# Performance work log

Hardware: AMD Instinct MI355X
Metric: run time of the kernel (lower is better)

Reference implementation:

```python
import jax, jax.numpy as jnp
import numpy as np

H, W = 96, 96
THRESHOLD = 0.9
C = 256

def setup_inputs() -> dict:
    key = jax.random.key(0)
    k1, k2 = jax.random.split(key)
    return {
        "feature_query": jax.random.normal(k1, (C, H, W), jnp.float32),
        "feature_projection": jax.random.normal(k2, (C, H, W), jnp.float32),
    }

def reference(feature_query, feature_projection):
    c = feature_query.shape[0]
    # flatten spatial dims -> [C, N]; L2-normalize each pixel's descriptor over channels
    q = feature_query.reshape(c, -1)
    p = feature_projection.reshape(c, -1)
    q = q / jnp.linalg.norm(q, axis=0, keepdims=True)
    p = p / jnp.linalg.norm(p, axis=0, keepdims=True)
    # cosine similarity matrix [N, M] (GEMM)
    sim = jnp.einsum('cn,cm->nm', q, p)
    col_max = jnp.argmax(sim, axis=0)   # [M] best query row per projection column
    row_max = jnp.argmax(sim, axis=1)   # [N] best projection column per query row
    j = jnp.arange(sim.shape[1])
    q_idx = col_max                      # candidate query index for each column j
    sim_vals = sim[q_idx, j]
    # mutual nearest-neighbor + threshold (fixed-shape boolean mask instead of
    # a data-dependent python list, for jit compatibility)
    mutual = (row_max[q_idx] == j) & (sim_vals > THRESHOLD)
    # oneDim2TwoDim: (idx // W, idx % W), valid only if div+1 < H
    q_div, q_mod = q_idx // W, q_idx % W
    p_div, p_mod = j // W, j % W
    valid = mutual & (q_div + 1 < H) & (p_div + 1 < H)
    return sim, valid, q_idx, q_div, q_mod, p_div, p_mod
```

## Files before the change

### kernel.cpp

```cpp
#include <hip/hip_runtime.h>
#include <hip/hip_fp16.h>

#define N_PIX 9216
#define CCH 256
#define W_ 96
#define H_ 96
#define BM 128
#define BN 128
#define BK 16
#define TM 8
#define TN 8

typedef _Float16 half8_t __attribute__((ext_vector_type(8)));
typedef float f32x4_t __attribute__((ext_vector_type(4)));

__device__ __forceinline__ unsigned int mono_enc(float f) {
    unsigned int u = __float_as_uint(f);
    return (u & 0x80000000u) ? ~u : (u | 0x80000000u);
}
__device__ __forceinline__ float mono_dec(unsigned int e) {
    return __uint_as_float((e & 0x80000000u) ? (e ^ 0x80000000u) : ~e);
}

__device__ __forceinline__ void gload_lds16(const uint4* g, uint4* lds) {
    __builtin_amdgcn_global_load_lds(
        (const __attribute__((address_space(1))) unsigned int*)g,
        (__attribute__((address_space(3))) unsigned int*)lds, 16, 0, 0);
}


__global__ __launch_bounds__(256) void norms_kernel(const float* __restrict__ Q,
                                                    const float* __restrict__ P,
                                                    float* __restrict__ invq,
                                                    float* __restrict__ invp) {
    int n = blockIdx.x * blockDim.x + threadIdx.x;
    if (n >= N_PIX) return;
    float sq = 0.f, sp = 0.f;
    for (int c = 0; c < CCH; ++c) {
        float a = Q[(size_t)c * N_PIX + n];
        float b = P[(size_t)c * N_PIX + n];
        sq = fmaf(a, a, sq);
        sp = fmaf(b, b, sp);
    }
    invq[n] = 1.0f / sqrtf(sq);
    invp[n] = 1.0f / sqrtf(sp);
}

__device__ __forceinline__ int local_row(int ty, int i) {
    return (i < 4) ? (ty * 4 + i) : (64 + ty * 4 + (i - 4));
}
__device__ __forceinline__ int local_col(int tx, int j) {
    return (j < 4) ? (tx * 4 + j) : (64 + tx * 4 + (j - 4));
}

__global__ __launch_bounds__(256) void gemm_kernel(const float* __restrict__ Q,
                                                   const float* __restrict__ P,
                                                   const float* __restrict__ invq,
                                                   const float* __restrict__ invp,
                                                   float* __restrict__ sim,
                                                   unsigned long long* __restrict__ row_best,
                                                   unsigned long long* __restrict__ col_best) {
    __shared__ union SH {
        struct { float A[BK][BM]; float B[BK][BN]; } t;
        unsigned long long red[16][128];
    } sh;

    const int tid = threadIdx.x;
    const int tx = tid & 15;
    const int ty = tid >> 4;
    const int n0 = blockIdx.y * BM;
    const int m0 = blockIdx.x * BN;

    float acc[TM][TN];
#pragma unroll
    for (int i = 0; i < TM; ++i)
#pragma unroll
        for (int j = 0; j < TN; ++j) acc[i][j] = 0.f;

    for (int kk = 0; kk < CCH; kk += BK) {
#pragma unroll
        for (int rep = 0; rep < 2; ++rep) {
            int idx = tid + rep * 256;
            int row = idx >> 5;
            int c4  = idx & 31;
            float4 av = *(const float4*)&Q[(size_t)(kk + row) * N_PIX + n0 + c4 * 4];
            float4 bv = *(const float4*)&P[(size_t)(kk + row) * N_PIX + m0 + c4 * 4];
            *(float4*)&sh.t.A[row][c4 * 4] = av;
            *(float4*)&sh.t.B[row][c4 * 4] = bv;
        }
        __syncthreads();
#pragma unroll
        for (int k = 0; k < BK; ++k) {
            float a[TM], b[TN];
            *(float4*)&a[0] = *(const float4*)&sh.t.A[k][ty * 4];
            *(float4*)&a[4] = *(const float4*)&sh.t.A[k][ty * 4 + 64];
            *(float4*)&b[0] = *(const float4*)&sh.t.B[k][tx * 4];
            *(float4*)&b[4] = *(const float4*)&sh.t.B[k][tx * 4 + 64];
#pragma unroll
            for (int i = 0; i < TM; ++i)
#pragma unroll
                for (int j = 0; j < TN; ++j)
                    acc[i][j] = fmaf(a[i], b[j], acc[i][j]);
        }
        __syncthreads();
    }

    float iq[TM], ip[TN];
#pragma unroll
    for (int i = 0; i < TM; ++i) iq[i] = invq[n0 + local_row(ty, i)];
#pragma unroll
    for (int j = 0; j < TN; ++j) ip[j] = invp[m0 + local_col(tx, j)];
#pragma unroll
    for (int i = 0; i < TM; ++i)
#pragma unroll
        for (int j = 0; j < TN; ++j) acc[i][j] *= iq[i] * ip[j];

#pragma unroll
    for (int i = 0; i < TM; ++i) {
        int n = n0 + local_row(ty, i);
        float4 v0 = make_float4(acc[i][0], acc[i][1], acc[i][2], acc[i][3]);
        float4 v1 = make_float4(acc[i][4], acc[i][5], acc[i][6], acc[i][7]);
        float* dst = &sim[(size_t)n * N_PIX + m0];
        *(float4*)(dst + tx * 4) = v0;
        *(float4*)(dst + 64 + tx * 4) = v1;
    }

#pragma unroll
    for (int i = 0; i < TM; ++i) {
        float best = acc[i][0]; int bj = 0;
#pragma unroll
        for (int j = 1; j < TN; ++j)
            if (acc[i][j] > best) { best = acc[i][j]; bj = j; }
        unsigned int gcol = (unsigned int)(m0 + local_col(tx, bj));
        sh.red[tx][local_row(ty, i)] =
            ((unsigned long long)mono_enc(best) << 32) | (unsigned long long)(0xFFFFFFFFu - gcol);
    }
    __syncthreads();
    if (tid < 128) {
        unsigned long long best = sh.red[0][tid];
#pragma unroll
        for (int x = 1; x < 16; ++x) {
            unsigned long long v = sh.red[x][tid];
            if (v > best) best = v;
        }
        atomicMax(&row_best[n0 + tid], best);
    }
    __syncthreads();

#pragma unroll
    for (int j = 0; j < TN; ++j) {
        float best = acc[0][j]; int bi = 0;
#pragma unroll
        for (int i = 1; i < TM; ++i)
            if (acc[i][j] > best) { best = acc[i][j]; bi = i; }
        unsigned int grow = (unsigned int)(n0 + local_row(ty, bi));
        sh.red[ty][local_col(tx, j)] =
            ((unsigned long long)mono_enc(best) << 32) | (unsigned long long)(0xFFFFFFFFu - grow);
    }
    __syncthreads();
    if (tid < 128) {
        unsigned long long best = sh.red[0][tid];
#pragma unroll
        for (int x = 1; x < 16; ++x) {
            unsigned long long v = sh.red[x][tid];
            if (v > best) best = v;
        }
        atomicMax(&col_best[m0 + tid], best);
    }
}


__device__ __forceinline__ unsigned int pack_pair(float x, float y, float& rx, float& ry) {
    __half hx = __float2half(x), hy = __float2half(y);
    rx = x - __half2float(hx);
    ry = y - __half2float(hy);
    return (unsigned int)__half_as_ushort(hx) | ((unsigned int)__half_as_ushort(hy) << 16);
}

__global__ __launch_bounds__(256) void prep_kernel(const float* __restrict__ Q,
                                                   const float* __restrict__ P,
                                                   uint4* __restrict__ qh,
                                                   uint4* __restrict__ ql,
                                                   uint4* __restrict__ ph,
                                                   uint4* __restrict__ pl,
                                                   float* __restrict__ invq,
                                                   float* __restrict__ invp) {
    __shared__ float rq[4][64];
    __shared__ float rp[4][64];
    const int lane = threadIdx.x & 63;
    const int band = threadIdx.x >> 6;
    const int n = blockIdx.x * 64 + lane;
    float sq = 0.f, sp = 0.f;
    for (int kb = band * 8; kb < band * 8 + 8; ++kb) {
        float a[8], b[8];
#pragma unroll
        for (int t = 0; t < 8; ++t) {
            a[t] = Q[(size_t)(kb * 8 + t) * N_PIX + n];
            b[t] = P[(size_t)(kb * 8 + t) * N_PIX + n];
        }
#pragma unroll
        for (int t = 0; t < 8; ++t) {
            sq = fmaf(a[t], a[t], sq);
            sp = fmaf(b[t], b[t], sp);
        }
        uint4 vqh, vql, vph, vpl;
        unsigned int* uqh = (unsigned int*)&vqh;
        unsigned int* uql = (unsigned int*)&vql;
        unsigned int* uph = (unsigned int*)&vph;
        unsigned int* upl = (unsigned int*)&vpl;
#pragma unroll
        for (int j = 0; j < 4; ++j) {
            float r0, r1;
            uqh[j] = pack_pair(a[2 * j], a[2 * j + 1], r0, r1);
            uql[j] = (unsigned int)__half_as_ushort(__float2half(r0))
                   | ((unsigned int)__half_as_ushort(__float2half(r1)) << 16);
            uph[j] = pack_pair(b[2 * j], b[2 * j + 1], r0, r1);
            upl[j] = (unsigned int)__half_as_ushort(__float2half(r0))
                   | ((unsigned int)__half_as_ushort(__float2half(r1)) << 16);
        }
        size_t o = (size_t)kb * N_PIX + n;
        qh[o] = vqh; ql[o] = vql; ph[o] = vph; pl[o] = vpl;
    }
    rq[band][lane] = sq;
    rp[band][lane] = sp;
    __syncthreads();
    if (threadIdx.x < 64) {
        float tq = rq[0][lane] + rq[1][lane] + rq[2][lane] + rq[3][lane];
        float tp = rp[0][lane] + rp[1][lane] + rp[2][lane] + rp[3][lane];
        invq[n] = 1.0f / sqrtf(tq);
        invp[n] = 1.0f / sqrtf(tp);
    }
}

__global__ __launch_bounds__(256, 2) void mfma_gemm_kernel(
        const uint4* __restrict__ QH, const uint4* __restrict__ QL,
        const uint4* __restrict__ PH, const uint4* __restrict__ PL,
        const float* __restrict__ invq, const float* __restrict__ invp,
        float* __restrict__ sim,
        unsigned long long* __restrict__ row_best,
        unsigned long long* __restrict__ col_best) {
    const unsigned int bid = blockIdx.x;
    const unsigned int xcd = bid & 7u;
    const unsigned int nbl = bid >> 3;
    const unsigned int gg  = nbl / 72u;
    const unsigned int rr  = nbl % 72u;
    const unsigned int by  = xcd * 9u + (rr >> 3);
    const unsigned int bx  = gg * 8u + (rr & 7u);

    const int tid = threadIdx.x;
    const int l  = tid & 63;
    const int w  = tid >> 6;
    const int rl = l & 15;
    const int kg = l >> 4;
    const int n0 = (int)by * 128;
    const int m0 = (int)bx * 128;
    const int r0 = n0 + (w >> 1) * 64;
    const int c0 = m0 + (w & 1) * 64;

    __shared__ union SH2 {
        uint4 stage[2][4][4][128];
        float st[4][16][68];
    } sh;

    const f32x4_t zero4 = {0.f, 0.f, 0.f, 0.f};
    f32x4_t acc[4][4];
#pragma unroll
    for (int i = 0; i < 4; ++i)
#pragma unroll
        for (int j = 0; j < 4; ++j) acc[i][j] = zero4;

    const uint4* gsrc = (w == 0) ? (QH + n0) : (w == 1) ? (QL + n0)
                      : (w == 2) ? (PH + m0) : (PL + m0);

#pragma unroll
    for (int kb = 0; kb < 4; ++kb)
#pragma unroll
        for (int h = 0; h < 2; ++h)
            gload_lds16(gsrc + (size_t)kb * N_PIX + h * 64 + l,
                        &sh.stage[0][w][kb][h * 64]);
    asm volatile("s_waitcnt vmcnt(0)" ::: "memory");
    __syncthreads();

    const int ar = (w >> 1) * 64 + rl;
    const int br = (w & 1) * 64 + rl;

    for (int s = 0; s < 8; ++s) {
        const int cur = s & 1;
        if (s < 7) {
            const uint4* gs = gsrc + (size_t)((s + 1) * 4) * N_PIX;
#pragma unroll
            for (int kb = 0; kb < 4; ++kb)
#pragma unroll
                for (int h = 0; h < 2; ++h)
                    gload_lds16(gs + (size_t)kb * N_PIX + h * 64 + l,
                                &sh.stage[cur ^ 1][w][kb][h * 64]);
        }
        half8_t ah[4], al4[4], bh4[4], bl4[4];
#pragma unroll
        for (int f = 0; f < 4; ++f) {
            ah[f]  = *(const half8_t*)&sh.stage[cur][0][kg][ar + f * 16];
            al4[f] = *(const half8_t*)&sh.stage[cur][1][kg][ar + f * 16];
            bh4[f] = *(const half8_t*)&sh.stage[cur][2][kg][br + f * 16];
            bl4[f] = *(const half8_t*)&sh.stage[cur][3][kg][br + f * 16];
        }
#pragma unroll
        for (int fr = 0; fr < 4; ++fr)
#pragma unroll
            for (int fc = 0; fc < 4; ++fc) {
                acc[fr][fc] = __builtin_amdgcn_mfma_f32_16x16x32_f16(ah[fr],  bh4[fc], acc[fr][fc], 0, 0, 0);
                acc[fr][fc] = __builtin_amdgcn_mfma_f32_16x16x32_f16(ah[fr],  bl4[fc], acc[fr][fc], 0, 0, 0);
                acc[fr][fc] = __builtin_amdgcn_mfma_f32_16x16x32_f16(al4[fr], bh4[fc], acc[fr][fc], 0, 0, 0);
            }
        asm volatile("s_waitcnt vmcnt(0)" ::: "memory");
        __syncthreads();
    }

    float iq[4][4];
#pragma unroll
    for (int fr = 0; fr < 4; ++fr) {
        const float4 v = *(const float4*)&invq[r0 + fr * 16 + kg * 4];
        iq[fr][0] = v.x; iq[fr][1] = v.y; iq[fr][2] = v.z; iq[fr][3] = v.w;
    }
    float ip[4];
#pragma unroll
    for (int fc = 0; fc < 4; ++fc) ip[fc] = invp[c0 + fc * 16 + rl];

#pragma unroll
    for (int fr = 0; fr < 4; ++fr)
#pragma unroll
        for (int fc = 0; fc < 4; ++fc)
#pragma unroll
            for (int j = 0; j < 4; ++j)
                acc[fr][fc][j] *= iq[fr][j] * ip[fc];

#pragma unroll
    for (int fr = 0; fr < 4; ++fr)
#pragma unroll
        for (int j = 0; j < 4; ++j) {
            float best = acc[fr][0][j];
            int bf = 0;
#pragma unroll
            for (int fc = 1; fc < 4; ++fc)
                if (acc[fr][fc][j] > best) { best = acc[fr][fc][j]; bf = fc; }
            const unsigned int gcol = (unsigned int)(c0 + bf * 16 + rl);
            unsigned long long key = ((unsigned long long)mono_enc(best) << 32)
                                   | (unsigned long long)(0xFFFFFFFFu - gcol);
#pragma unroll
            for (int m = 1; m < 16; m <<= 1) {
                unsigned long long o = __shfl_xor(key, m, 64);
                if (o > key) key = o;
            }
            if (rl == 0)
                atomicMax(&row_best[r0 + fr * 16 + kg * 4 + j], key);
        }

#pragma unroll
    for (int fc = 0; fc < 4; ++fc) {
        float best = acc[0][fc][0];
        unsigned int brow = (unsigned int)(r0 + kg * 4);
#pragma unroll
        for (int fr = 0; fr < 4; ++fr)
#pragma unroll
            for (int j = 0; j < 4; ++j) {
                float v = acc[fr][fc][j];
                unsigned int rr2 = (unsigned int)(r0 + fr * 16 + kg * 4 + j);
                if (v > best) { best = v; brow = rr2; }
            }
        unsigned long long key = ((unsigned long long)mono_enc(best) << 32)
                               | (unsigned long long)(0xFFFFFFFFu - brow);
#pragma unroll
        for (int m = 16; m < 64; m <<= 1) {
            unsigned long long o = __shfl_xor(key, m, 64);
            if (o > key) key = o;
        }
        if (kg == 0)
            atomicMax(&col_best[c0 + fc * 16 + rl], key);
    }

#pragma unroll
    for (int fr = 0; fr < 4; ++fr) {
        asm volatile("s_waitcnt lgkmcnt(0)" ::: "memory");
#pragma unroll
        for (int fc = 0; fc < 4; ++fc)
#pragma unroll
            for (int j = 0; j < 4; ++j)
                sh.st[w][kg * 4 + j][fc * 16 + rl] = acc[fr][fc][j];
        asm volatile("s_waitcnt lgkmcnt(0)" ::: "memory");
#pragma unroll
        for (int pass = 0; pass < 4; ++pass) {
            const int rowL = pass * 4 + kg;
            const f32x4_t v = *(const f32x4_t*)&sh.st[w][rowL][rl * 4];
            const int gr = r0 + fr * 16 + rowL;
            __builtin_nontemporal_store(v, (f32x4_t*)(sim + (size_t)gr * N_PIX + c0 + rl * 4));
        }
    }
}


__global__ __launch_bounds__(256) void epilogue_kernel(const unsigned long long* __restrict__ row_best,
                                                       const unsigned long long* __restrict__ col_best,
                                                       float* __restrict__ out) {
    int j = blockIdx.x * blockDim.x + threadIdx.x;
    if (j >= N_PIX) return;
    unsigned long long cb = col_best[j];
    unsigned int q_idx = 0xFFFFFFFFu - (unsigned int)(cb & 0xFFFFFFFFull);
    float simval = mono_dec((unsigned int)(cb >> 32));
    unsigned long long rb = row_best[q_idx];
    unsigned int rm = 0xFFFFFFFFu - (unsigned int)(rb & 0xFFFFFFFFull);
    bool mutual = (rm == (unsigned int)j) && (simval > 0.9f);
    int qd = (int)(q_idx / W_), qm = (int)(q_idx % W_);
    int pd = j / W_, pm = j % W_;
    bool valid = mutual && (qd + 1 < H_) && (pd + 1 < H_);
    size_t base = (size_t)N_PIX * N_PIX;
    out[base + 0 * (size_t)N_PIX + j] = valid ? 1.0f : 0.0f;
    out[base + 1 * (size_t)N_PIX + j] = (float)q_idx;
    out[base + 2 * (size_t)N_PIX + j] = (float)qd;
    out[base + 3 * (size_t)N_PIX + j] = (float)qm;
    out[base + 4 * (size_t)N_PIX + j] = (float)pd;
    out[base + 5 * (size_t)N_PIX + j] = (float)pm;
}

extern "C" void kernel_launch(void* const* d_in, const int* in_sizes, int n_in,
                              void* d_out, int out_size, void* d_ws, size_t ws_size,
                              hipStream_t stream) {
    const float* Q = (const float*)d_in[0];
    const float* P = (const float*)d_in[1];
    float* out = (float*)d_out;

    unsigned long long* row_best = (unsigned long long*)d_ws;
    unsigned long long* col_best = row_best + N_PIX;
    float* invq = (float*)(col_best + N_PIX);
    float* invp = invq + N_PIX;

    hipMemsetAsync(d_ws, 0, 2 * N_PIX * sizeof(unsigned long long), stream);

    const size_t base_bytes = 2 * N_PIX * sizeof(unsigned long long) + 2 * N_PIX * sizeof(float);
    const size_t arr_u4 = (size_t)(CCH / 8) * N_PIX;
    const size_t need = base_bytes + 4 * arr_u4 * sizeof(uint4);

    if (ws_size >= need) {
        uint4* qh = (uint4*)((char*)d_ws + base_bytes);
        uint4* ql = qh + arr_u4;
        uint4* ph = ql + arr_u4;
        uint4* pl = ph + arr_u4;

        prep_kernel<<<N_PIX / 64, 256, 0, stream>>>(Q, P, qh, ql, ph, pl, invq, invp);
        mfma_gemm_kernel<<<5184, 256, 0, stream>>>(qh, ql, ph, pl, invq, invp,
                                                   out, row_best, col_best);
    } else {
        norms_kernel<<<N_PIX / 256, 256, 0, stream>>>(Q, P, invq, invp);
        dim3 grid(N_PIX / BN, N_PIX / BM);
        gemm_kernel<<<grid, 256, 0, stream>>>(Q, P, invq, invp, out, row_best, col_best);
    }

    epilogue_kernel<<<N_PIX / 256, 256, 0, stream>>>(row_best, col_best, out);
}
```

Baseline: 467.9 us.

## Enlarge GEMM tiles to 192x192 with 8 waves and triple-buffered LDS staging

Grows the block tile from 128x128 to 192x192 and the block from 256 to 512 threads, with each wave computing a 48x96 sub-tile (3x6 MFMA fragments). Staging becomes a three-deep LDS ring with partial vmcnt waits, so two K-steps of global loads are in flight while computing. The block-to-XCD mapping and the grid size change to match. The aim is more data reuse per load and better overlap of loads with MFMA work, at the cost of more LDS, more registers per thread and a grid of 2304 blocks that may fill the CUs less evenly.

```diff
diff --git a/kernel.cpp b/kernel.cpp
--- a/kernel.cpp
+++ b/kernel.cpp
@@ -232,7 +232,7 @@
     }
 }
 
-__global__ __launch_bounds__(256, 2) void mfma_gemm_kernel(
+__global__ __launch_bounds__(512, 2) void mfma_gemm_kernel(
         const uint4* __restrict__ QH, const uint4* __restrict__ QL,
         const uint4* __restrict__ PH, const uint4* __restrict__ PL,
         const float* __restrict__ invq, const float* __restrict__ invp,
@@ -242,105 +242,119 @@
     const unsigned int bid = blockIdx.x;
     const unsigned int xcd = bid & 7u;
     const unsigned int nbl = bid >> 3;
-    const unsigned int gg  = nbl / 72u;
-    const unsigned int rr  = nbl % 72u;
-    const unsigned int by  = xcd * 9u + (rr >> 3);
-    const unsigned int bx  = gg * 8u + (rr & 7u);
+    const unsigned int g   = nbl >> 3;
+    const unsigned int ii  = nbl & 7u;
+    const unsigned int by  = xcd * 6u + g % 6u;
+    const unsigned int bx  = (g / 6u) * 8u + ii;
 
     const int tid = threadIdx.x;
     const int l  = tid & 63;
     const int w  = tid >> 6;
     const int rl = l & 15;
     const int kg = l >> 4;
-    const int n0 = (int)by * 128;
-    const int m0 = (int)bx * 128;
-    const int r0 = n0 + (w >> 1) * 64;
-    const int c0 = m0 + (w & 1) * 64;
+    const int wr = w >> 1;
+    const int wc = w & 1;
+    const int n0 = (int)by * 192;
+    const int m0 = (int)bx * 192;
+    const int r0 = n0 + wr * 48;
+    const int c0 = m0 + wc * 96;
 
     __shared__ union SH2 {
-        uint4 stage[2][4][4][128];
-        float st[4][16][68];
+        uint4 stage[3][4][4][192];
+        float st[8][16][108];
     } sh;
 
     const f32x4_t zero4 = {0.f, 0.f, 0.f, 0.f};
-    f32x4_t acc[4][4];
-#pragma unroll
-    for (int i = 0; i < 4; ++i)
-#pragma unroll
-        for (int j = 0; j < 4; ++j) acc[i][j] = zero4;
-
-    const uint4* gsrc = (w == 0) ? (QH + n0) : (w == 1) ? (QL + n0)
-                      : (w == 2) ? (PH + m0) : (PL + m0);
-
-#pragma unroll
-    for (int kb = 0; kb < 4; ++kb)
-#pragma unroll
-        for (int h = 0; h < 2; ++h)
-            gload_lds16(gsrc + (size_t)kb * N_PIX + h * 64 + l,
-                        &sh.stage[0][w][kb][h * 64]);
-    asm volatile("s_waitcnt vmcnt(0)" ::: "memory");
-    __syncthreads();
-
-    const int ar = (w >> 1) * 64 + rl;
-    const int br = (w & 1) * 64 + rl;
-
+    f32x4_t acc[3][6];
+#pragma unroll
+    for (int i = 0; i < 3; ++i)
+#pragma unroll
+        for (int j = 0; j < 6; ++j) acc[i][j] = zero4;
+
+    const int h3  = w >> 2;
+    const int arr = w & 3;
+    const uint4* gsrc = (arr == 0) ? (QH + n0) : (arr == 1) ? (QL + n0)
+                      : (arr == 2) ? (PH + m0) : (PL + m0);
+
+#define STAGE(step, buf)                                                        \
+    {                                                                           \
+        _Pragma("unroll")                                                       \
+        for (int i = 0; i < 6; ++i) {                                           \
+            const int rest = 2 * i + h3;                                        \
+            const int kb = rest & 3;                                            \
+            const int px0 = (rest >> 2) * 64;                                   \
+            gload_lds16(gsrc + (size_t)((step) * 4 + kb) * N_PIX + px0 + l,     \
+                        &sh.stage[buf][arr][kb][px0]);                          \
+        }                                                                       \
+    }
+
+    STAGE(0, 0)
+    STAGE(1, 1)
+    asm volatile("s_waitcnt vmcnt(6)" ::: "memory");
+    __builtin_amdgcn_s_barrier();
+    __builtin_amdgcn_sched_barrier(0);
+
+#pragma unroll
     for (int s = 0; s < 8; ++s) {
-        const int cur = s & 1;
-        if (s < 7) {
-            const uint4* gs = gsrc + (size_t)((s + 1) * 4) * N_PIX;
-#pragma unroll
-            for (int kb = 0; kb < 4; ++kb)
-#pragma unroll
-                for (int h = 0; h < 2; ++h)
-                    gload_lds16(gs + (size_t)kb * N_PIX + h * 64 + l,
-                                &sh.stage[cur ^ 1][w][kb][h * 64]);
-        }
-        half8_t ah[4], al4[4], bh4[4], bl4[4];
-#pragma unroll
-        for (int f = 0; f < 4; ++f) {
-            ah[f]  = *(const half8_t*)&sh.stage[cur][0][kg][ar + f * 16];
-            al4[f] = *(const half8_t*)&sh.stage[cur][1][kg][ar + f * 16];
-            bh4[f] = *(const half8_t*)&sh.stage[cur][2][kg][br + f * 16];
-            bl4[f] = *(const half8_t*)&sh.stage[cur][3][kg][br + f * 16];
-        }
-#pragma unroll
-        for (int fr = 0; fr < 4; ++fr)
-#pragma unroll
-            for (int fc = 0; fc < 4; ++fc) {
-                acc[fr][fc] = __builtin_amdgcn_mfma_f32_16x16x32_f16(ah[fr],  bh4[fc], acc[fr][fc], 0, 0, 0);
-                acc[fr][fc] = __builtin_amdgcn_mfma_f32_16x16x32_f16(ah[fr],  bl4[fc], acc[fr][fc], 0, 0, 0);
-                acc[fr][fc] = __builtin_amdgcn_mfma_f32_16x16x32_f16(al4[fr], bh4[fc], acc[fr][fc], 0, 0, 0);
+        const int cur = s % 3;
+        if (s < 6) STAGE(s + 2, (s + 2) % 3)
+
+        half8_t ah[3], al_[3], bh_[6], bl_[6];
+#pragma unroll
+        for (int f = 0; f < 3; ++f) {
+            ah[f]  = *(const half8_t*)&sh.stage[cur][0][kg][wr * 48 + f * 16 + rl];
+            al_[f] = *(const half8_t*)&sh.stage[cur][1][kg][wr * 48 + f * 16 + rl];
+        }
+#pragma unroll
+        for (int f = 0; f < 6; ++f) {
+            bh_[f] = *(const half8_t*)&sh.stage[cur][2][kg][wc * 96 + f * 16 + rl];
+            bl_[f] = *(const half8_t*)&sh.stage[cur][3][kg][wc * 96 + f * 16 + rl];
+        }
+#pragma unroll
+        for (int fr = 0; fr < 3; ++fr)
+#pragma unroll
+            for (int fc = 0; fc < 6; ++fc) {
+                acc[fr][fc] = __builtin_amdgcn_mfma_f32_16x16x32_f16(ah[fr],  bh_[fc], acc[fr][fc], 0, 0, 0);
+                acc[fr][fc] = __builtin_amdgcn_mfma_f32_16x16x32_f16(ah[fr],  bl_[fc], acc[fr][fc], 0, 0, 0);
+                acc[fr][fc] = __builtin_amdgcn_mfma_f32_16x16x32_f16(al_[fr], bh_[fc], acc[fr][fc], 0, 0, 0);
             }
-        asm volatile("s_waitcnt vmcnt(0)" ::: "memory");
-        __syncthreads();
-    }
-
-    float iq[4][4];
-#pragma unroll
-    for (int fr = 0; fr < 4; ++fr) {
+
+        if (s < 6) {
+            asm volatile("s_waitcnt vmcnt(6)" ::: "memory");
+        } else if (s == 6) {
+            asm volatile("s_waitcnt vmcnt(0)" ::: "memory");
+        }
+        __builtin_amdgcn_s_barrier();
+        __builtin_amdgcn_sched_barrier(0);
+    }
+#undef STAGE
+
+    float iq[3][4];
+#pragma unroll
+    for (int fr = 0; fr < 3; ++fr) {
         const float4 v = *(const float4*)&invq[r0 + fr * 16 + kg * 4];
         iq[fr][0] = v.x; iq[fr][1] = v.y; iq[fr][2] = v.z; iq[fr][3] = v.w;
     }
-    float ip[4];
-#pragma unroll
-    for (int fc = 0; fc < 4; ++fc) ip[fc] = invp[c0 + fc * 16 + rl];
-
-#pragma unroll
-    for (int fr = 0; fr < 4; ++fr)
-#pragma unroll
-        for (int fc = 0; fc < 4; ++fc)
+    float ip[6];
+#pragma unroll
+    for (int fc = 0; fc < 6; ++fc) ip[fc] = invp[c0 + fc * 16 + rl];
+
+#pragma unroll
+    for (int fr = 0; fr < 3; ++fr)
+#pragma unroll
+        for (int fc = 0; fc < 6; ++fc)
 #pragma unroll
             for (int j = 0; j < 4; ++j)
                 acc[fr][fc][j] *= iq[fr][j] * ip[fc];
 
 #pragma unroll
-    for (int fr = 0; fr < 4; ++fr)
+    for (int fr = 0; fr < 3; ++fr)
 #pragma unroll
         for (int j = 0; j < 4; ++j) {
             float best = acc[fr][0][j];
             int bf = 0;
 #pragma unroll
-            for (int fc = 1; fc < 4; ++fc)
+            for (int fc = 1; fc < 6; ++fc)
                 if (acc[fr][fc][j] > best) { best = acc[fr][fc][j]; bf = fc; }
             const unsigned int gcol = (unsigned int)(c0 + bf * 16 + rl);
             unsigned long long key = ((unsigned long long)mono_enc(best) << 32)
@@ -355,11 +369,11 @@
         }
 
 #pragma unroll
-    for (int fc = 0; fc < 4; ++fc) {
+    for (int fc = 0; fc < 6; ++fc) {
         float best = acc[0][fc][0];
         unsigned int brow = (unsigned int)(r0 + kg * 4);
 #pragma unroll
-        for (int fr = 0; fr < 4; ++fr)
+        for (int fr = 0; fr < 3; ++fr)
 #pragma unroll
             for (int j = 0; j < 4; ++j) {
                 float v = acc[fr][fc][j];
@@ -378,20 +392,22 @@
     }
 
 #pragma unroll
-    for (int fr = 0; fr < 4; ++fr) {
+    for (int fr = 0; fr < 3; ++fr) {
         asm volatile("s_waitcnt lgkmcnt(0)" ::: "memory");
 #pragma unroll
-        for (int fc = 0; fc < 4; ++fc)
+        for (int fc = 0; fc < 6; ++fc)
 #pragma unroll
             for (int j = 0; j < 4; ++j)
                 sh.st[w][kg * 4 + j][fc * 16 + rl] = acc[fr][fc][j];
         asm volatile("s_waitcnt lgkmcnt(0)" ::: "memory");
 #pragma unroll
-        for (int pass = 0; pass < 4; ++pass) {
-            const int rowL = pass * 4 + kg;
-            const f32x4_t v = *(const f32x4_t*)&sh.st[w][rowL][rl * 4];
-            const int gr = r0 + fr * 16 + rowL;
-            __builtin_nontemporal_store(v, (f32x4_t*)(sim + (size_t)gr * N_PIX + c0 + rl * 4));
+        for (int p = 0; p < 6; ++p) {
+            const int flat = p * 64 + l;
+            const int row = flat / 24;
+            const int c4  = flat % 24;
+            const f32x4_t v = *(const f32x4_t*)&sh.st[w][row][c4 * 4];
+            const int gr = r0 + fr * 16 + row;
+            __builtin_nontemporal_store(v, (f32x4_t*)(sim + (size_t)gr * N_PIX + c0 + c4 * 4));
         }
     }
 }
@@ -445,7 +461,7 @@
         uint4* pl = ph + arr_u4;
 
         prep_kernel<<<N_PIX / 64, 256, 0, stream>>>(Q, P, qh, ql, ph, pl, invq, invp);
-        mfma_gemm_kernel<<<5184, 256, 0, stream>>>(qh, ql, ph, pl, invq, invp,
+        mfma_gemm_kernel<<<2304, 512, 0, stream>>>(qh, ql, ph, pl, invq, invp,
                                                    out, row_best, col_best);
     } else {
         norms_kernel<<<N_PIX / 256, 256, 0, stream>>>(Q, P, invq, invp);
```

Result: slower. 485.8 us (+3.8%).

## Load A fragments directly to registers, triple-buffer B in LDS, fuse workspace zeroing

Applied to the files above, without the earlier changes.

The GEMM main loop no longer stages the Q hi/lo fragments through LDS. Each wave loads its A fragments straight from global memory into double-buffered registers, while only the P hi/lo tiles go through a three-stage LDS ring using partial vmcnt waits, so fewer full drains are needed per iteration. MFMA sections are wrapped in s_setprio. The prep kernel now uses more, smaller blocks and also zeroes the row/col best buffers, which removes the separate memset launch. The risks are more redundant global loads of A across waves, higher register pressure, and the correctness of the manual wait counts.

```diff
diff --git a/kernel.cpp b/kernel.cpp
--- a/kernel.cpp
+++ b/kernel.cpp
@@ -184,24 +184,31 @@
                                                    uint4* __restrict__ ph,
                                                    uint4* __restrict__ pl,
                                                    float* __restrict__ invq,
-                                                   float* __restrict__ invp) {
-    __shared__ float rq[4][64];
-    __shared__ float rp[4][64];
-    const int lane = threadIdx.x & 63;
-    const int band = threadIdx.x >> 6;
-    const int n = blockIdx.x * 64 + lane;
+                                                   float* __restrict__ invp,
+                                                   unsigned long long* __restrict__ best01) {
+    __shared__ float rq[16][17];
+    __shared__ float rp[16][17];
+    const int t = threadIdx.x;
+    const int n16 = t & 15;
+    const int ks = t >> 4;
+    const int n = blockIdx.x * 16 + n16;
+
+    if (t < 32) best01[blockIdx.x * 32 + t] = 0ULL;
+
     float sq = 0.f, sp = 0.f;
-    for (int kb = band * 8; kb < band * 8 + 8; ++kb) {
+#pragma unroll
+    for (int kk = 0; kk < 2; ++kk) {
+        const int kb = ks * 2 + kk;
         float a[8], b[8];
 #pragma unroll
-        for (int t = 0; t < 8; ++t) {
-            a[t] = Q[(size_t)(kb * 8 + t) * N_PIX + n];
-            b[t] = P[(size_t)(kb * 8 + t) * N_PIX + n];
-        }
-#pragma unroll
-        for (int t = 0; t < 8; ++t) {
-            sq = fmaf(a[t], a[t], sq);
-            sp = fmaf(b[t], b[t], sp);
+        for (int u = 0; u < 8; ++u) {
+            a[u] = Q[(size_t)(kb * 8 + u) * N_PIX + n];
+            b[u] = P[(size_t)(kb * 8 + u) * N_PIX + n];
+        }
+#pragma unroll
+        for (int u = 0; u < 8; ++u) {
+            sq = fmaf(a[u], a[u], sq);
+            sp = fmaf(b[u], b[u], sp);
         }
         uint4 vqh, vql, vph, vpl;
         unsigned int* uqh = (unsigned int*)&vqh;
@@ -221,14 +228,20 @@
         size_t o = (size_t)kb * N_PIX + n;
         qh[o] = vqh; ql[o] = vql; ph[o] = vph; pl[o] = vpl;
     }
-    rq[band][lane] = sq;
-    rp[band][lane] = sp;
+    rq[ks][n16] = sq;
+    rp[ks][n16] = sp;
     __syncthreads();
-    if (threadIdx.x < 64) {
-        float tq = rq[0][lane] + rq[1][lane] + rq[2][lane] + rq[3][lane];
-        float tp = rp[0][lane] + rp[1][lane] + rp[2][lane] + rp[3][lane];
-        invq[n] = 1.0f / sqrtf(tq);
-        invp[n] = 1.0f / sqrtf(tp);
+    if (t < 16) {
+        float s = 0.f;
+#pragma unroll
+        for (int x = 0; x < 16; ++x) s += rq[x][t];
+        invq[blockIdx.x * 16 + t] = 1.0f / sqrtf(s);
+    } else if (t < 32) {
+        const int tt = t - 16;
+        float s = 0.f;
+#pragma unroll
+        for (int x = 0; x < 16; ++x) s += rp[x][tt];
+        invp[blockIdx.x * 16 + tt] = 1.0f / sqrtf(s);
     }
 }
 
@@ -258,62 +271,82 @@
     const int c0 = m0 + (w & 1) * 64;
 
     __shared__ union SH2 {
-        uint4 stage[2][4][4][128];
+        uint4 bstage[3][2][4][128];
         float st[4][16][68];
     } sh;
 
-    const f32x4_t zero4 = {0.f, 0.f, 0.f, 0.f};
     f32x4_t acc[4][4];
 #pragma unroll
     for (int i = 0; i < 4; ++i)
 #pragma unroll
-        for (int j = 0; j < 4; ++j) acc[i][j] = zero4;
-
-    const uint4* gsrc = (w == 0) ? (QH + n0) : (w == 1) ? (QL + n0)
-                      : (w == 2) ? (PH + m0) : (PL + m0);
-
-#pragma unroll
-    for (int kb = 0; kb < 4; ++kb)
-#pragma unroll
-        for (int h = 0; h < 2; ++h)
-            gload_lds16(gsrc + (size_t)kb * N_PIX + h * 64 + l,
-                        &sh.stage[0][w][kb][h * 64]);
-    asm volatile("s_waitcnt vmcnt(0)" ::: "memory");
-    __syncthreads();
-
-    const int ar = (w >> 1) * 64 + rl;
-    const int br = (w & 1) * 64 + rl;
-
+        for (int j = 0; j < 4; ++j) acc[i][j] = {0.f, 0.f, 0.f, 0.f};
+
+    const int sarr  = w & 1;
+    const int shalf = w >> 1;
+    const uint4* bptr = ((sarr == 0) ? PH : PL) + m0 + shalf * 64;
+
+#define BSTAGE(t_, b_)                                                          \
+    {                                                                           \
+        _Pragma("unroll")                                                       \
+        for (int kb = 0; kb < 4; ++kb)                                          \
+            gload_lds16(bptr + (size_t)((t_) * 4 + kb) * N_PIX + l,             \
+                        &sh.bstage[b_][sarr][kb][shalf * 64]);                  \
+    }
+
+    union Frag { uint4 u; half8_t h; };
+    Frag ahA[4], alA[4], ahB[4], alB[4];
+    const uint4* qhp = QH + r0 + rl;
+    const uint4* qlp = QL + r0 + rl;
+
+#define ALOAD(t_, dh_, dl_)                                                     \
+    {                                                                           \
+        _Pragma("unroll")                                                       \
+        for (int f = 0; f < 4; ++f) {                                           \
+            dh_[f].u = qhp[(size_t)((t_) * 4 + kg) * N_PIX + f * 16];           \
+            dl_[f].u = qlp[(size_t)((t_) * 4 + kg) * N_PIX + f * 16];           \
+        }                                                                       \
+    }
+
+    BSTAGE(0, 0)
+    BSTAGE(1, 1)
+    ALOAD(0, ahA, alA)
+    asm volatile("s_waitcnt vmcnt(12)" ::: "memory");
+    __builtin_amdgcn_s_barrier();
+    __builtin_amdgcn_sched_barrier(0);
+
+#pragma unroll
     for (int s = 0; s < 8; ++s) {
-        const int cur = s & 1;
+        if (s < 6) BSTAGE(s + 2, (s + 2) % 3)
         if (s < 7) {
-            const uint4* gs = gsrc + (size_t)((s + 1) * 4) * N_PIX;
-#pragma unroll
-            for (int kb = 0; kb < 4; ++kb)
-#pragma unroll
-                for (int h = 0; h < 2; ++h)
-                    gload_lds16(gs + (size_t)kb * N_PIX + h * 64 + l,
-                                &sh.stage[cur ^ 1][w][kb][h * 64]);
-        }
-        half8_t ah[4], al4[4], bh4[4], bl4[4];
+            if (s & 1) { ALOAD(s + 1, ahA, alA) }
+            else       { ALOAD(s + 1, ahB, alB) }
+        }
+        Frag (&ah)[4] = (s & 1) ? ahB : ahA;
+        Frag (&al)[4] = (s & 1) ? alB : alA;
+
+        half8_t bh_[4], bl_[4];
 #pragma unroll
         for (int f = 0; f < 4; ++f) {
-            ah[f]  = *(const half8_t*)&sh.stage[cur][0][kg][ar + f * 16];
-            al4[f] = *(const half8_t*)&sh.stage[cur][1][kg][ar + f * 16];
-            bh4[f] = *(const half8_t*)&sh.stage[cur][2][kg][br + f * 16];
-            bl4[f] = *(const half8_t*)&sh.stage[cur][3][kg][br + f * 16];
-        }
+            bh_[f] = *(const half8_t*)&sh.bstage[s % 3][0][kg][(w & 1) * 64 + f * 16 + rl];
+            bl_[f] = *(const half8_t*)&sh.bstage[s % 3][1][kg][(w & 1) * 64 + f * 16 + rl];
+        }
+
+        __builtin_amdgcn_s_setprio(1);
 #pragma unroll
         for (int fr = 0; fr < 4; ++fr)
 #pragma unroll
             for (int fc = 0; fc < 4; ++fc) {
-                acc[fr][fc] = __builtin_amdgcn_mfma_f32_16x16x32_f16(ah[fr],  bh4[fc], acc[fr][fc], 0, 0, 0);
-                acc[fr][fc] = __builtin_amdgcn_mfma_f32_16x16x32_f16(ah[fr],  bl4[fc], acc[fr][fc], 0, 0, 0);
-                acc[fr][fc] = __builtin_amdgcn_mfma_f32_16x16x32_f16(al4[fr], bh4[fc], acc[fr][fc], 0, 0, 0);
+                acc[fr][fc] = __builtin_amdgcn_mfma_f32_16x16x32_f16(ah[fr].h, bh_[fc], acc[fr][fc], 0, 0, 0);
+                acc[fr][fc] = __builtin_amdgcn_mfma_f32_16x16x32_f16(ah[fr].h, bl_[fc], acc[fr][fc], 0, 0, 0);
+                acc[fr][fc] = __builtin_amdgcn_mfma_f32_16x16x32_f16(al[fr].h, bh_[fc], acc[fr][fc], 0, 0, 0);
             }
-        asm volatile("s_waitcnt vmcnt(0)" ::: "memory");
-        __syncthreads();
-    }
+        __builtin_amdgcn_s_setprio(0);
+
+        __builtin_amdgcn_s_barrier();
+        __builtin_amdgcn_sched_barrier(0);
+    }
+#undef BSTAGE
+#undef ALOAD
 
     float iq[4][4];
 #pragma unroll
@@ -432,8 +465,6 @@
     float* invq = (float*)(col_best + N_PIX);
     float* invp = invq + N_PIX;
 
-    hipMemsetAsync(d_ws, 0, 2 * N_PIX * sizeof(unsigned long long), stream);
-
     const size_t base_bytes = 2 * N_PIX * sizeof(unsigned long long) + 2 * N_PIX * sizeof(float);
     const size_t arr_u4 = (size_t)(CCH / 8) * N_PIX;
     const size_t need = base_bytes + 4 * arr_u4 * sizeof(uint4);
@@ -444,10 +475,12 @@
         uint4* ph = ql + arr_u4;
         uint4* pl = ph + arr_u4;
 
-        prep_kernel<<<N_PIX / 64, 256, 0, stream>>>(Q, P, qh, ql, ph, pl, invq, invp);
+        prep_kernel<<<N_PIX / 16, 256, 0, stream>>>(Q, P, qh, ql, ph, pl, invq, invp,
+                                                    (unsigned long long*)d_ws);
         mfma_gemm_kernel<<<5184, 256, 0, stream>>>(qh, ql, ph, pl, invq, invp,
                                                    out, row_best, col_best);
     } else {
+        hipMemsetAsync(d_ws, 0, 2 * N_PIX * sizeof(unsigned long long), stream);
         norms_kernel<<<N_PIX / 256, 256, 0, stream>>>(Q, P, invq, invp);
         dim3 grid(N_PIX / BN, N_PIX / BM);
         gemm_kernel<<<grid, 256, 0, stream>>>(Q, P, invq, invp, out, row_best, col_best);
```

New measurement: 472.2 us. No clear change (+0.9%).
